# Kernel optimization log

Measured on AMD Instinct MI355X. Metric: run time of the kernel, lower is better.

Reference implementation:

```python
import jax, jax.numpy as jnp
import numpy as np

# Architecture constants (from init_kwargs)
A, L, NCF = 200, 10, 9            # num_agent, in_len, num_control_features
D_MODEL, N_HEADS = 1024, 4
HEAD_DIM = D_MODEL // N_HEADS      # 256 (the module's 'head_dim')
PER_HEAD = HEAD_DIM // N_HEADS     # 64 (effective per-head dim after rearrange)
SCALE = HEAD_DIM ** -0.5           # module scales by head_dim**-0.5
N = A * L + NCF                    # 2009 tokens


def _build_mask():
    # block-diagonal agent mask: eye(A) repeat_interleaved L on both axes,
    # then zero-padded by NCF rows/cols for control features
    m = np.kron(np.eye(A, dtype=np.float32), np.ones((L, L), dtype=np.float32))
    m = np.pad(m, ((0, NCF), (0, NCF)))
    return jnp.asarray(m)  # [N, N]

_MASK = _build_mask()


def setup_inputs() -> dict:
    key = jax.random.key(0)
    k0, k1, k2, k3 = jax.random.split(key, 4)
    x = jax.random.normal(k0, (4, N, D_MODEL), jnp.float32)
    W_qkv = jax.random.normal(k1, (D_MODEL, HEAD_DIM * 3), jnp.float32) * 0.02
    W_qk_self = jax.random.normal(k2, (D_MODEL, HEAD_DIM * 2), jnp.float32) * 0.02
    W_out = jax.random.normal(k3, (HEAD_DIM, D_MODEL), jnp.float32) * 0.02
    b_out = jnp.zeros((D_MODEL,), jnp.float32)
    return {"x": x, "W_qkv": W_qkv, "W_qk_self": W_qk_self,
            "W_out": W_out, "b_out": b_out}


def _heads(t, b, n):
    # 'b n (h d) -> b h n d' with h = N_HEADS
    return t.reshape(b, n, N_HEADS, PER_HEAD).transpose(0, 2, 1, 3)


def reference(x, W_qkv, W_qk_self, W_out, b_out):
    b, n, _ = x.shape
    q, k, v = jnp.split(x @ W_qkv, 3, axis=-1)          # each [b, n, HEAD_DIM]
    q, k, v = _heads(q, b, n), _heads(k, b, n), _heads(v, b, n)  # [b,h,n,d]
    q_self, k_self = jnp.split(x @ W_qk_self, 2, axis=-1)
    q_self, k_self = _heads(q_self, b, n), _heads(k_self, b, n)

    dots = jnp.einsum('bhnd,bhmd->bhnm', q, k) * SCALE
    dots_self = jnp.einsum('bhnd,bhmd->bhnm', q_self, k_self) * SCALE
    dots_all = _MASK * dots_self + (1.0 - _MASK) * dots  # blend via block mask
    attn = jax.nn.softmax(dots_all, axis=-1)             # [b,h,n,n]

    out = jnp.einsum('bhnm,bhmd->bhnd', attn, v)
    out = out.transpose(0, 2, 1, 3).reshape(b, n, HEAD_DIM)  # 'b h n d -> b n (h d)'
    out = out @ W_out + b_out                            # to_out (dropout=0)
    return out, attn
```

## Files before the change

### kernel.cpp

```cpp
#include <hip/hip_runtime.h>

typedef unsigned short u16;
typedef unsigned int u32;
typedef short short8 __attribute__((ext_vector_type(8)));
typedef float f32x4 __attribute__((ext_vector_type(4)));
typedef float f32x16 __attribute__((ext_vector_type(16)));
typedef float float4a __attribute__((ext_vector_type(4), aligned(4)));

#define NTOK 2009
#define M8   8036
#define DMOD 1024
#define PKBH 129024

static __device__ __forceinline__ u16 f2bf(float f) {
  unsigned int x = __float_as_uint(f);
  x += 0x7fffu + ((x >> 16) & 1u);
  return (u16)(x >> 16);
}
static __device__ __forceinline__ float bf2f(u16 u) {
  return __uint_as_float((unsigned int)u << 16);
}
static __device__ __forceinline__ u32 pk2(float a, float b) {
  return (u32)f2bf(a) | ((u32)f2bf(b) << 16);
}
static __device__ __forceinline__ u32 cvtpk(float a, float b) {
  u32 d;
  asm("v_cvt_pk_bf16_f32 %0, %1, %2" : "=v"(d) : "v"(a), "v"(b));
  return d;
}
static __device__ __forceinline__ void gload_lds16(const void* g, void* l) {
  __builtin_amdgcn_global_load_lds(
      (const __attribute__((address_space(1))) void*)g,
      (__attribute__((address_space(3))) void*)l, 16, 0, 0);
}

__global__ void k_conv_x(const float* __restrict__ x, u16* __restrict__ xb) {
  int i = blockIdx.x * 256 + threadIdx.x;
  float4 v = ((const float4*)x)[i];
  unsigned int a = (unsigned int)f2bf(v.x) | ((unsigned int)f2bf(v.y) << 16);
  unsigned int b = (unsigned int)f2bf(v.z) | ((unsigned int)f2bf(v.w) << 16);
  ((uint2*)xb)[i] = make_uint2(a, b);
}

__global__ void k_conv_wcat(const float* __restrict__ Wqkv, const float* __restrict__ Wqs,
                            u16* __restrict__ WtCat) {
  int i = blockIdx.x * 256 + threadIdx.x;
  int n = i >> 10, k = i & 1023;
  float v = (n < 768) ? Wqkv[k * 768 + n] : Wqs[k * 512 + (n - 768)];
  WtCat[i] = f2bf(v);
}

__global__ void k_conv_wout(const float* __restrict__ Wout, u16* __restrict__ WtOut) {
  int i = blockIdx.x * 256 + threadIdx.x;
  int n = i >> 8, k = i & 255;
  WtOut[i] = f2bf(Wout[k * 1024 + n]);
}

__global__ __launch_bounds__(256) void k_gemm_proj(
    const u16* __restrict__ A, const u16* __restrict__ Bt,
    u16* __restrict__ Qp, u16* __restrict__ Kp, u16* __restrict__ Vp,
    u16* __restrict__ Qsb, u16* __restrict__ Ksb)
{
  __shared__ u16 Asm[128 * 64];
  __shared__ u16 Bsm[128 * 64];
  int mt = blockIdx.x * 128, nt = blockIdx.y * 128;
  int tid = threadIdx.x, lane = tid & 63, w = tid >> 6;
  int wm = w >> 1, wn = w & 1;
  int fr = lane & 15, fq = lane >> 4;
  int srow = w * 32 + (lane >> 3);
  int scol = (lane & 7) * 8;
  f32x4 acc[4][4];
#pragma unroll
  for (int a = 0; a < 4; ++a)
#pragma unroll
    for (int b = 0; b < 4; ++b) acc[a][b] = (f32x4){0.f, 0.f, 0.f, 0.f};

  for (int kt = 0; kt < 1024; kt += 64) {
#pragma unroll
    for (int j = 0; j < 4; ++j) {
      int r = srow + j * 8;
      int am = mt + r; if (am >= M8) am = 0;
      gload_lds16(A + (size_t)am * 1024 + kt + scol, Asm + (size_t)(w * 32 + j * 8) * 64);
      gload_lds16(Bt + (size_t)(nt + r) * 1024 + kt + scol, Bsm + (size_t)(w * 32 + j * 8) * 64);
    }
    __syncthreads();
#pragma unroll
    for (int cs = 0; cs < 2; ++cs) {
      short8 af[4], bf[4];
#pragma unroll
      for (int i = 0; i < 4; ++i) {
        af[i] = *(const short8*)&Asm[(size_t)(wm * 64 + i * 16 + fr) * 64 + cs * 32 + fq * 8];
        bf[i] = *(const short8*)&Bsm[(size_t)(wn * 64 + i * 16 + fr) * 64 + cs * 32 + fq * 8];
      }
#pragma unroll
      for (int mi = 0; mi < 4; ++mi)
#pragma unroll
        for (int ni = 0; ni < 4; ++ni)
          acc[mi][ni] = __builtin_amdgcn_mfma_f32_16x16x32_bf16(af[mi], bf[ni], acc[mi][ni], 0, 0, 0);
    }
    __syncthreads();
  }

#pragma unroll
  for (int ni = 0; ni < 4; ++ni) {
    int n = nt + wn * 64 + ni * 16 + fr;
    int g = n >> 6, d = n & 63;
    int h = g & 3, sel = g >> 2;
    float scl = (sel == 0 || sel == 3) ? 0.0625f : 1.0f;
#pragma unroll
    for (int mi = 0; mi < 4; ++mi) {
#pragma unroll
      for (int i = 0; i < 4; ++i) {
        int m = mt + wm * 64 + mi * 16 + fq * 4 + i;
        if (m >= M8) continue;
        int b_ = m / NTOK, tok = m - b_ * NTOK;
        int bh = b_ * 4 + h;
        u16 val = f2bf(acc[mi][ni][i] * scl);
        if (sel <= 1) {
          u16* dst = sel == 0 ? Qp : Kp;
          size_t idx = ((((size_t)bh * 63 + (tok >> 5)) * 4 + (d >> 4)) * 2 + ((d >> 3) & 1)) * 256
                       + (tok & 31) * 8 + (d & 7);
          dst[idx] = val;
        } else if (sel == 2) {
          size_t idx = (((((size_t)bh * 63 + (tok >> 5)) * 2 + (d >> 5)) * 2 + ((tok >> 4) & 1)) * 2
                        + ((tok >> 3) & 1)) * 256 + (d & 31) * 8 + (tok & 7);
          Vp[idx] = val;
        } else {
          u16* p = (sel == 3) ? Qsb : Ksb;
          p[((size_t)bh * NTOK + tok) * 64 + d] = val;
        }
      }
    }
  }
}

__global__ void k_self(const u16* __restrict__ Qs, const u16* __restrict__ Ks,
                       float* __restrict__ selfS) {
  int blk = blockIdx.x;
  int bh = blk / 200, a = blk % 200;
  int t = threadIdx.x;
  if (t >= 100) return;
  int ri = t / 10, rj = t % 10;
  const u16* qp = &Qs[((size_t)bh * NTOK + a * 10 + ri) * 64];
  const u16* kp = &Ks[((size_t)bh * NTOK + a * 10 + rj) * 64];
  float s = 0.f;
#pragma unroll 8
  for (int k = 0; k < 64; ++k) s += bf2f(qp[k]) * bf2f(kp[k]);
  selfS[(size_t)blk * 100 + t] = s;
}

__global__ __launch_bounds__(256, 2) void k_attn8(
    const u16* __restrict__ Qp, const u16* __restrict__ Kp,
    const u16* __restrict__ Vp, const float* __restrict__ selfS,
    float* __restrict__ attn, u16* __restrict__ Ob)
{
  __shared__ float s_sum[4][32];
  __shared__ float s_o[4][64][32];
  __shared__ float s_p[4][1024];
  int bh = blockIdx.x;
  int qt = blockIdx.y;
  int q0 = qt * 32;
  int tid = threadIdx.x;
  int lane = tid & 63, w = tid >> 6;
  int ql = lane & 31, h = lane >> 5;
  int qg = q0 + ql;
  int lo8 = ql * 8;

  const u16* qbase = Qp + (size_t)bh * PKBH + (size_t)qt * 2048;
  const u16* kbase = Kp + (size_t)bh * PKBH;
  const u16* vbase = Vp + (size_t)bh * PKBH;

  short8 qf[4];
#pragma unroll
  for (int c = 0; c < 4; ++c)
    qf[c] = *(const short8*)&qbase[(c * 2 + h) * 256 + lo8];

  int qa = (qg < 2000) ? (qg / 10) : -1;
  int band_lo = 1 << 30, band_hi = -(1 << 30);
  if (q0 < 2000) {
    int hi_row = (q0 + 31 < 1999) ? q0 + 31 : 1999;
    band_lo = (q0 / 10) * 10;
    band_hi = (hi_row / 10) * 10 + 10;
  }
  const float* sfb = &selfS[(size_t)bh * 20000];

  int t0 = w * 16;
  int t1 = t0 + 16; if (t1 > 63) t1 = 63;

  u32 pb[16][8];
  short8 kf[4], kfn[4], vf[4];
  f32x16 oacc0 = {}, oacc1 = {};

#pragma unroll
  for (int c = 0; c < 4; ++c)
    kf[c] = *(const short8*)&kbase[(size_t)t0 * 2048 + (c * 2 + h) * 256 + lo8];
  float ssum = 0.f;
#pragma unroll
  for (int i = 0; i < 16; ++i) {
    int t = t0 + i;
    if (t < t1) {
      int tn = (t + 1 < t1) ? t + 1 : t0;
#pragma unroll
      for (int c = 0; c < 4; ++c)
        vf[c] = *(const short8*)&vbase[(size_t)t * 2048 + (c * 2 + h) * 256 + lo8];
#pragma unroll
      for (int c = 0; c < 4; ++c)
        kfn[c] = *(const short8*)&kbase[(size_t)tn * 2048 + (c * 2 + h) * 256 + lo8];
      f32x16 acc = {};
#pragma unroll
      for (int c = 0; c < 4; ++c)
        acc = __builtin_amdgcn_mfma_f32_32x32x16_bf16(kf[c], qf[c], acc, 0, 0, 0);
      int kt = t * 32;
      float e[16];
      if ((kt < band_hi) && (kt + 32 > band_lo)) {
#pragma unroll
        for (int r = 0; r < 16; ++r) {
          int kc = kt + (r & 3) + 8 * (r >> 2) + 4 * h;
          float sc = acc[r];
          if (qa >= 0 && kc < 2000 && (kc / 10) == qa)
            sc = sfb[qa * 100 + (qg - qa * 10) * 10 + (kc - qa * 10)];
          e[r] = __expf(sc);
        }
      } else {
#pragma unroll
        for (int r = 0; r < 16; ++r) e[r] = __expf(acc[r]);
      }
      if (t == 62) {
#pragma unroll
        for (int r = 0; r < 16; ++r) {
          int kc = kt + (r & 3) + 8 * (r >> 2) + 4 * h;
          if (kc >= NTOK) e[r] = 0.f;
        }
      }
#pragma unroll
      for (int r2 = 0; r2 < 8; ++r2) {
        pb[i][r2] = cvtpk(e[2 * r2], e[2 * r2 + 1]);
        ssum += e[2 * r2] + e[2 * r2 + 1];
      }
      u32 p00 = __shfl_xor(pb[i][0], 32), p01 = __shfl_xor(pb[i][1], 32);
      u32 p10 = __shfl_xor(pb[i][2], 32), p11 = __shfl_xor(pb[i][3], 32);
      u32 p20 = __shfl_xor(pb[i][4], 32), p21 = __shfl_xor(pb[i][5], 32);
      u32 p30 = __shfl_xor(pb[i][6], 32), p31 = __shfl_xor(pb[i][7], 32);
      u32 b0[4], b1[4];
      b0[0] = h ? p10 : pb[i][0];  b0[1] = h ? p11 : pb[i][1];
      b0[2] = h ? pb[i][2] : p00;  b0[3] = h ? pb[i][3] : p01;
      b1[0] = h ? p30 : pb[i][4];  b1[1] = h ? p31 : pb[i][5];
      b1[2] = h ? pb[i][6] : p20;  b1[3] = h ? pb[i][7] : p21;
      short8 B0, B1;
      __builtin_memcpy(&B0, b0, 16);
      __builtin_memcpy(&B1, b1, 16);
      oacc0 = __builtin_amdgcn_mfma_f32_32x32x16_bf16(vf[0], B0, oacc0, 0, 0, 0);
      oacc1 = __builtin_amdgcn_mfma_f32_32x32x16_bf16(vf[2], B0, oacc1, 0, 0, 0);
      oacc0 = __builtin_amdgcn_mfma_f32_32x32x16_bf16(vf[1], B1, oacc0, 0, 0, 0);
      oacc1 = __builtin_amdgcn_mfma_f32_32x32x16_bf16(vf[3], B1, oacc1, 0, 0, 0);
#pragma unroll
      for (int c = 0; c < 4; ++c) kf[c] = kfn[c];
    }
  }
  ssum += __shfl_xor(ssum, 32);
  if (lane < 32) s_sum[w][ql] = ssum;
  __syncthreads();
  float inv = 1.0f / (s_sum[0][ql] + s_sum[1][ql] + s_sum[2][ql] + s_sum[3][ql]);

  char* pl = (char*)&s_p[w][0];
#pragma unroll
  for (int i = 0; i < 16; ++i) {
    int t = t0 + i;
    if (t < t1) {
      int kt = t * 32;
#pragma unroll
      for (int rq = 0; rq < 4; ++rq) {
        u32 ua = pb[i][2 * rq], ub = pb[i][2 * rq + 1];
        f32x4 v = {__uint_as_float(ua << 16) * inv,
                   __uint_as_float(ua & 0xffff0000u) * inv,
                   __uint_as_float(ub << 16) * inv,
                   __uint_as_float(ub & 0xffff0000u) * inv};
        *(f32x4*)(pl + ql * 128 + ((rq * 32 + h * 16) ^ ((ql & 7) << 4))) = v;
      }
#pragma unroll
      for (int i2 = 0; i2 < 4; ++i2) {
        int r = i2 * 8 + (lane >> 3), ch = lane & 7;
        f32x4 v = *(f32x4*)(pl + r * 128 + ((ch * 16) ^ ((r & 7) << 4)));
        int grow = q0 + r;
        int col0 = kt + ch * 4;
        if (grow < NTOK) {
          float* arow = &attn[((size_t)bh * NTOK + grow) * NTOK];
          if (col0 + 3 < NTOK) {
            *(float4a*)&arow[col0] = (float4a){v[0], v[1], v[2], v[3]};
          } else {
#pragma unroll
            for (int j = 0; j < 4; ++j)
              if (col0 + j < NTOK) arow[col0 + j] = v[j];
          }
        }
      }
    }
  }

#pragma unroll
  for (int r = 0; r < 16; ++r) {
    int d = (r & 3) + 8 * (r >> 2) + 4 * h;
    s_o[w][d][ql] = oacc0[r];
    s_o[w][d + 32][ql] = oacc1[r];
  }
  __syncthreads();
  {
    int q = tid & 31, dg = tid >> 5;
    int qg2 = q0 + q;
    if (qg2 < NTOK) {
      float invq = 1.0f / (s_sum[0][q] + s_sum[1][q] + s_sum[2][q] + s_sum[3][q]);
      int b_ = bh >> 2, hd = bh & 3;
      u16* orow = &Ob[((size_t)(b_ * NTOK + qg2)) * 256 + hd * 64 + dg * 8];
      u32 wpk[4];
#pragma unroll
      for (int j = 0; j < 4; ++j) {
        int d = dg * 8 + 2 * j;
        float a = (s_o[0][d][q] + s_o[1][d][q] + s_o[2][d][q] + s_o[3][d][q]) * invq;
        float b = (s_o[0][d + 1][q] + s_o[1][d + 1][q] + s_o[2][d + 1][q] + s_o[3][d + 1][q]) * invq;
        wpk[j] = pk2(a, b);
      }
      *(uint4*)orow = make_uint4(wpk[0], wpk[1], wpk[2], wpk[3]);
    }
  }
}

__global__ __launch_bounds__(256) void k_gemm_out(
    const u16* __restrict__ A, const u16* __restrict__ Bt,
    const float* __restrict__ bias, float* __restrict__ C)
{
  __shared__ u16 Asm[128 * 64];
  __shared__ u16 Bsm[128 * 64];
  int mt = blockIdx.x * 128, nt = blockIdx.y * 128;
  int tid = threadIdx.x, lane = tid & 63, w = tid >> 6;
  int wm = w >> 1, wn = w & 1;
  int fr = lane & 15, fq = lane >> 4;
  int srow = w * 32 + (lane >> 3);
  int scol = (lane & 7) * 8;
  f32x4 acc[4][4];
#pragma unroll
  for (int a = 0; a < 4; ++a)
#pragma unroll
    for (int b = 0; b < 4; ++b) acc[a][b] = (f32x4){0.f, 0.f, 0.f, 0.f};

  for (int kt = 0; kt < 256; kt += 64) {
#pragma unroll
    for (int j = 0; j < 4; ++j) {
      int r = srow + j * 8;
      int am = mt + r; if (am >= M8) am = 0;
      gload_lds16(A + (size_t)am * 256 + kt + scol, Asm + (size_t)(w * 32 + j * 8) * 64);
      gload_lds16(Bt + (size_t)(nt + r) * 256 + kt + scol, Bsm + (size_t)(w * 32 + j * 8) * 64);
    }
    __syncthreads();
#pragma unroll
    for (int cs = 0; cs < 2; ++cs) {
      short8 af[4], bf[4];
#pragma unroll
      for (int i = 0; i < 4; ++i) {
        af[i] = *(const short8*)&Asm[(size_t)(wm * 64 + i * 16 + fr) * 64 + cs * 32 + fq * 8];
        bf[i] = *(const short8*)&Bsm[(size_t)(wn * 64 + i * 16 + fr) * 64 + cs * 32 + fq * 8];
      }
#pragma unroll
      for (int mi = 0; mi < 4; ++mi)
#pragma unroll
        for (int ni = 0; ni < 4; ++ni)
          acc[mi][ni] = __builtin_amdgcn_mfma_f32_16x16x32_bf16(af[mi], bf[ni], acc[mi][ni], 0, 0, 0);
    }
    __syncthreads();
  }

#pragma unroll
  for (int ni = 0; ni < 4; ++ni) {
    int n = nt + wn * 64 + ni * 16 + fr;
    float bn = bias[n];
#pragma unroll
    for (int mi = 0; mi < 4; ++mi)
#pragma unroll
      for (int i = 0; i < 4; ++i) {
        int m = mt + wm * 64 + mi * 16 + fq * 4 + i;
        if (m < M8) C[(size_t)m * DMOD + n] = acc[mi][ni][i] + bn;
      }
  }
}

extern "C" void kernel_launch(void* const* d_in, const int* in_sizes, int n_in,
                              void* d_out, int out_size, void* d_ws, size_t ws_size,
                              hipStream_t stream) {
  (void)in_sizes; (void)n_in; (void)out_size; (void)ws_size;
  const float* x    = (const float*)d_in[0];
  const float* Wqkv = (const float*)d_in[1];
  const float* Wqs  = (const float*)d_in[2];
  const float* Wout = (const float*)d_in[3];
  const float* bout = (const float*)d_in[4];
  float* out  = (float*)d_out;
  float* attn = out + (size_t)M8 * DMOD;

  char* ws = (char*)d_ws;
  u16*   xb    = (u16*)(ws);
  u16*   WtCat = (u16*)(ws + 16457728);
  u16*   WtOut = (u16*)(ws + 19079168);
  u16*   Qp    = (u16*)(ws + 19603456);
  u16*   Kp    = (u16*)(ws + 23732224);
  u16*   Vp    = (u16*)(ws + 27860992);
  u16*   Qsb   = (u16*)(ws + 31989760);
  u16*   Ksb   = (u16*)(ws + 36104192);
  u16*   Ob    = (u16*)(ws + 40218624);
  float* selfS = (float*)(ws + 44333056);

  k_conv_x<<<dim3(8036), dim3(256), 0, stream>>>(x, xb);
  k_conv_wcat<<<dim3(5120), dim3(256), 0, stream>>>(Wqkv, Wqs, WtCat);
  k_conv_wout<<<dim3(1024), dim3(256), 0, stream>>>(Wout, WtOut);
  k_gemm_proj<<<dim3(63, 10), dim3(256), 0, stream>>>(xb, WtCat, Qp, Kp, Vp, Qsb, Ksb);
  k_self<<<dim3(3200), dim3(128), 0, stream>>>(Qsb, Ksb, selfS);
  k_attn8<<<dim3(16, 63), dim3(256), 0, stream>>>(Qp, Kp, Vp, selfS, attn, Ob);
  k_gemm_out<<<dim3(63, 8), dim3(256), 0, stream>>>(Ob, WtOut, bout, out);
}
```

Measured before the change: 217.9 us.

## Merge conversion kernels and write attn rows directly without LDS transpose

Fuses the three fp32-to-bf16 conversion kernels into one launch using block-range dispatch, which removes two launch overheads. The attention kernel stops staging the probability tile through shared memory for a coalesced transpose. Each lane now writes its own row's float4 chunks straight to global memory, with a fast path for non-tail key tiles. This cuts LDS traffic and shared-memory footprint, but the attn stores become less coalesced: each lane writes 16-byte pieces spread across rows.

```diff
diff --git a/kernel.cpp b/kernel.cpp
--- a/kernel.cpp
+++ b/kernel.cpp
@@ -34,26 +34,27 @@
       (__attribute__((address_space(3))) void*)l, 16, 0, 0);
 }
 
-__global__ void k_conv_x(const float* __restrict__ x, u16* __restrict__ xb) {
-  int i = blockIdx.x * 256 + threadIdx.x;
-  float4 v = ((const float4*)x)[i];
-  unsigned int a = (unsigned int)f2bf(v.x) | ((unsigned int)f2bf(v.y) << 16);
-  unsigned int b = (unsigned int)f2bf(v.z) | ((unsigned int)f2bf(v.w) << 16);
-  ((uint2*)xb)[i] = make_uint2(a, b);
-}
-
-__global__ void k_conv_wcat(const float* __restrict__ Wqkv, const float* __restrict__ Wqs,
-                            u16* __restrict__ WtCat) {
-  int i = blockIdx.x * 256 + threadIdx.x;
-  int n = i >> 10, k = i & 1023;
-  float v = (n < 768) ? Wqkv[k * 768 + n] : Wqs[k * 512 + (n - 768)];
-  WtCat[i] = f2bf(v);
-}
-
-__global__ void k_conv_wout(const float* __restrict__ Wout, u16* __restrict__ WtOut) {
-  int i = blockIdx.x * 256 + threadIdx.x;
-  int n = i >> 8, k = i & 255;
-  WtOut[i] = f2bf(Wout[k * 1024 + n]);
+__global__ void k_convs(const float* __restrict__ x, u16* __restrict__ xb,
+                        const float* __restrict__ Wqkv, const float* __restrict__ Wqs,
+                        u16* __restrict__ WtCat,
+                        const float* __restrict__ Wout, u16* __restrict__ WtOut) {
+  int blk = blockIdx.x;
+  if (blk < 8036) {
+    int i = blk * 256 + threadIdx.x;
+    float4 v = ((const float4*)x)[i];
+    unsigned int a = (unsigned int)f2bf(v.x) | ((unsigned int)f2bf(v.y) << 16);
+    unsigned int b = (unsigned int)f2bf(v.z) | ((unsigned int)f2bf(v.w) << 16);
+    ((uint2*)xb)[i] = make_uint2(a, b);
+  } else if (blk < 8036 + 5120) {
+    int i = (blk - 8036) * 256 + threadIdx.x;
+    int n = i >> 10, k = i & 1023;
+    float v = (n < 768) ? Wqkv[k * 768 + n] : Wqs[k * 512 + (n - 768)];
+    WtCat[i] = f2bf(v);
+  } else {
+    int i = (blk - 8036 - 5120) * 256 + threadIdx.x;
+    int n = i >> 8, k = i & 255;
+    WtOut[i] = f2bf(Wout[k * 1024 + n]);
+  }
 }
 
 __global__ __launch_bounds__(256) void k_gemm_proj(
@@ -149,14 +150,13 @@
   selfS[(size_t)blk * 100 + t] = s;
 }
 
-__global__ __launch_bounds__(256, 2) void k_attn8(
+__global__ __launch_bounds__(256, 2) void k_attn13(
     const u16* __restrict__ Qp, const u16* __restrict__ Kp,
     const u16* __restrict__ Vp, const float* __restrict__ selfS,
     float* __restrict__ attn, u16* __restrict__ Ob)
 {
   __shared__ float s_sum[4][32];
   __shared__ float s_o[4][64][32];
-  __shared__ float s_p[4][1024];
   int bh = blockIdx.x;
   int qt = blockIdx.y;
   int q0 = qt * 32;
@@ -164,6 +164,8 @@
   int lane = tid & 63, w = tid >> 6;
   int ql = lane & 31, h = lane >> 5;
   int qg = q0 + ql;
+  bool qok = qg < NTOK;
+  int qc = qok ? qg : NTOK - 1;
   int lo8 = ql * 8;
 
   const u16* qbase = Qp + (size_t)bh * PKBH + (size_t)qt * 2048;
@@ -262,35 +264,37 @@
   __syncthreads();
   float inv = 1.0f / (s_sum[0][ql] + s_sum[1][ql] + s_sum[2][ql] + s_sum[3][ql]);
 
-  char* pl = (char*)&s_p[w][0];
+  float* arow = &attn[((size_t)bh * NTOK + qc) * NTOK];
 #pragma unroll
   for (int i = 0; i < 16; ++i) {
     int t = t0 + i;
-    if (t < t1) {
+    if (t < t1 && qok) {
       int kt = t * 32;
-#pragma unroll
-      for (int rq = 0; rq < 4; ++rq) {
-        u32 ua = pb[i][2 * rq], ub = pb[i][2 * rq + 1];
-        f32x4 v = {__uint_as_float(ua << 16) * inv,
-                   __uint_as_float(ua & 0xffff0000u) * inv,
-                   __uint_as_float(ub << 16) * inv,
-                   __uint_as_float(ub & 0xffff0000u) * inv};
-        *(f32x4*)(pl + ql * 128 + ((rq * 32 + h * 16) ^ ((ql & 7) << 4))) = v;
-      }
-#pragma unroll
-      for (int i2 = 0; i2 < 4; ++i2) {
-        int r = i2 * 8 + (lane >> 3), ch = lane & 7;
-        f32x4 v = *(f32x4*)(pl + r * 128 + ((ch * 16) ^ ((r & 7) << 4)));
-        int grow = q0 + r;
-        int col0 = kt + ch * 4;
-        if (grow < NTOK) {
-          float* arow = &attn[((size_t)bh * NTOK + grow) * NTOK];
+      float e[16];
+#pragma unroll
+      for (int r2 = 0; r2 < 8; ++r2) {
+        u32 u = pb[i][r2];
+        e[2 * r2]     = __uint_as_float(u << 16) * inv;
+        e[2 * r2 + 1] = __uint_as_float(u & 0xffff0000u) * inv;
+      }
+      if (t < 62) {
+#pragma unroll
+        for (int rq = 0; rq < 4; ++rq) {
+          int col0 = kt + 8 * rq + 4 * h;
+          *(float4a*)&arow[col0] =
+              (float4a){e[4 * rq], e[4 * rq + 1], e[4 * rq + 2], e[4 * rq + 3]};
+        }
+      } else {
+#pragma unroll
+        for (int rq = 0; rq < 4; ++rq) {
+          int col0 = kt + 8 * rq + 4 * h;
           if (col0 + 3 < NTOK) {
-            *(float4a*)&arow[col0] = (float4a){v[0], v[1], v[2], v[3]};
+            *(float4a*)&arow[col0] =
+                (float4a){e[4 * rq], e[4 * rq + 1], e[4 * rq + 2], e[4 * rq + 3]};
           } else {
 #pragma unroll
             for (int j = 0; j < 4; ++j)
-              if (col0 + j < NTOK) arow[col0 + j] = v[j];
+              if (col0 + j < NTOK) arow[col0 + j] = e[4 * rq + j];
           }
         }
       }
@@ -406,11 +410,10 @@
   u16*   Ob    = (u16*)(ws + 40218624);
   float* selfS = (float*)(ws + 44333056);
 
-  k_conv_x<<<dim3(8036), dim3(256), 0, stream>>>(x, xb);
-  k_conv_wcat<<<dim3(5120), dim3(256), 0, stream>>>(Wqkv, Wqs, WtCat);
-  k_conv_wout<<<dim3(1024), dim3(256), 0, stream>>>(Wout, WtOut);
+  k_convs<<<dim3(8036 + 5120 + 1024), dim3(256), 0, stream>>>(
+      x, xb, Wqkv, Wqs, WtCat, Wout, WtOut);
   k_gemm_proj<<<dim3(63, 10), dim3(256), 0, stream>>>(xb, WtCat, Qp, Kp, Vp, Qsb, Ksb);
   k_self<<<dim3(3200), dim3(128), 0, stream>>>(Qsb, Ksb, selfS);
-  k_attn8<<<dim3(16, 63), dim3(256), 0, stream>>>(Qp, Kp, Vp, selfS, attn, Ob);
+  k_attn13<<<dim3(16, 63), dim3(256), 0, stream>>>(Qp, Kp, Vp, selfS, attn, Ob);
   k_gemm_out<<<dim3(63, 8), dim3(256), 0, stream>>>(Ob, WtOut, bout, out);
 }
```

Measured after the change: 197.0 us. 9.6% less time.
